# Optimization experiments

Hardware: AMD Instinct MI355X
Metric: run time of the kernel (lower is better)

Reference implementation:

```python
import jax, jax.numpy as jnp
import numpy as np
import math

B, LC, LQ, D = 64, 1024, 128, 128


def setup_inputs() -> dict:
    key = jax.random.key(0)
    k1, k2, k3, k4, k5 = jax.random.split(key, 5)
    c_rep = jax.random.normal(k1, (B, LC, D), dtype=jnp.float32)
    q_rep = jax.random.normal(k2, (B, LQ, D), dtype=jnp.float32)
    c_mask = jax.random.randint(k3, (B, LC), 0, 2, dtype=jnp.int32)
    q_mask = jax.random.randint(k4, (B, LQ), 0, 2, dtype=jnp.int32)
    lim = math.sqrt(1.0 / D)
    w = jax.random.uniform(k5, (3 * D,), dtype=jnp.float32, minval=-lim, maxval=lim)
    return {"c_rep": c_rep, "q_rep": q_rep, "c_mask": c_mask, "q_mask": q_mask, "w": w}


def _mask_logits(t, m):
    # mask == 1 means masked (matches original: target*(1-mask) + mask*-1e30)
    return t * (1.0 - m) + m * (-1e30)


def reference(c_rep, q_rep, c_mask, q_mask, w):
    d = c_rep.shape[-1]
    w1, w2, w3 = w[:d], w[d:2 * d], w[2 * d:]
    # Trilinear similarity S[b,i,j] = <ct,w1> + <qt,w2> + <ct*qt,w3>
    # computed without materializing the [B,Lc,Lq,3D] concat tensor.
    S = (c_rep @ w1)[:, :, None] \
        + (q_rep @ w2)[:, None, :] \
        + jnp.einsum('bid,bjd->bij', c_rep * w3, q_rep)  # [B, Lc, Lq]
    qm = q_mask[:, None, :].astype(S.dtype)  # [B, 1, Lq]
    cm = c_mask[:, :, None].astype(S.dtype)  # [B, Lc, 1]
    S1 = jax.nn.softmax(_mask_logits(S, qm), axis=2)  # softmax over query dim
    S2 = jax.nn.softmax(_mask_logits(S, cm), axis=1)  # softmax over context dim
    A = jnp.einsum('bij,bjd->bid', S1, q_rep)  # [B, Lc, D]
    # B_att = S1 @ S2^T @ c_rep, associated right-first to avoid [B,Lc,Lc]
    T = jnp.einsum('bkj,bkd->bjd', S2, c_rep)  # [B, Lq, D]
    B_att = jnp.einsum('bij,bjd->bid', S1, T)  # [B, Lc, D]
    out = jnp.concatenate([c_rep, A, c_rep * A, c_rep * B_att], axis=2)  # [B, Lc, 4D]
    # dropout is identity at inference
    return out
```

## Files before the change

### kernel.cpp

```cpp
#include <hip/hip_runtime.h>
#include <hip/hip_bf16.h>
#include <cstdint>
#include <cstddef>

#define B_   64
#define LC_  1024
#define LQ_  128
#define D_   128

typedef __bf16 bf16;
typedef bf16  bf16x8 __attribute__((ext_vector_type(8)));
typedef bf16  bf16x4 __attribute__((ext_vector_type(4)));
typedef float f32x4  __attribute__((ext_vector_type(4)));

__device__ __forceinline__ f32x4 mfma16(bf16x8 a, bf16x8 b, f32x4 c) {
  return __builtin_amdgcn_mfma_f32_16x16x32_bf16(a, b, c, 0, 0, 0);
}

__global__ __launch_bounds__(256) void k0c(const float* __restrict__ c, const float* __restrict__ w,
                                           float* __restrict__ cw1, bf16* __restrict__ cw3,
                                           bf16* __restrict__ cT) {
  __shared__ float w1s[128];
  __shared__ float w3s[128];
  __shared__ bf16  ctile[128 * 132];
  const int b = blockIdx.y, ks = blockIdx.x;
  const int k0 = ks * 128;
  const int t = threadIdx.x;
  if (t < 128) { w1s[t] = w[t]; w3s[t] = w[256 + t]; }
  __syncthreads();
  {
    const int r = t >> 1, d0 = (t & 1) * 64;
    const float* crow = c + ((size_t)(b * LC_ + k0 + r) * D_ + d0);
    bf16* orow = cw3 + ((size_t)(b * LC_ + k0 + r) * D_ + d0);
    float dot = 0.f;
#pragma unroll
    for (int v = 0; v < 8; ++v) {
      const float4 f0 = ((const float4*)crow)[v * 2 + 0];
      const float4 f1 = ((const float4*)crow)[v * 2 + 1];
      const int dd = d0 + v * 8;
      dot += f0.x * w1s[dd + 0] + f0.y * w1s[dd + 1] + f0.z * w1s[dd + 2] + f0.w * w1s[dd + 3]
           + f1.x * w1s[dd + 4] + f1.y * w1s[dd + 5] + f1.z * w1s[dd + 6] + f1.w * w1s[dd + 7];
      bf16* cr = &ctile[r * 132 + dd];
      cr[0] = (bf16)f0.x; cr[1] = (bf16)f0.y; cr[2] = (bf16)f0.z; cr[3] = (bf16)f0.w;
      cr[4] = (bf16)f1.x; cr[5] = (bf16)f1.y; cr[6] = (bf16)f1.z; cr[7] = (bf16)f1.w;
      bf16x8 o;
      o[0] = (bf16)(f0.x * w3s[dd + 0]); o[1] = (bf16)(f0.y * w3s[dd + 1]);
      o[2] = (bf16)(f0.z * w3s[dd + 2]); o[3] = (bf16)(f0.w * w3s[dd + 3]);
      o[4] = (bf16)(f1.x * w3s[dd + 4]); o[5] = (bf16)(f1.y * w3s[dd + 5]);
      o[6] = (bf16)(f1.z * w3s[dd + 6]); o[7] = (bf16)(f1.w * w3s[dd + 7]);
      *(bf16x8*)(orow + v * 8) = o;
    }
    dot += __shfl_xor(dot, 1);
    if ((t & 1) == 0) cw1[b * LC_ + k0 + r] = dot;
  }
  __syncthreads();
  {
    const int d = t >> 1, kh = (t & 1) * 64;
    bf16* trow = cT + ((size_t)(b * D_ + d) * LC_ + k0 + kh);
#pragma unroll
    for (int v = 0; v < 8; ++v) {
      bf16x8 o;
#pragma unroll
      for (int e = 0; e < 8; ++e) o[e] = ctile[(kh + v * 8 + e) * 132 + d];
      *(bf16x8*)(trow + v * 8) = o;
    }
  }
}

__global__ __launch_bounds__(256) void k0q(const float* __restrict__ q, const float* __restrict__ w,
                                           float* __restrict__ qw2, bf16* __restrict__ qb,
                                           bf16* __restrict__ qT) {
  __shared__ float w2s[128];
  __shared__ bf16  qtile[128 * 132];
  const int b = blockIdx.x;
  const int t = threadIdx.x;
  if (t < 128) w2s[t] = w[128 + t];
  __syncthreads();
  {
    const int r = t >> 1, d0 = (t & 1) * 64;
    const float* qrow = q + ((size_t)(b * LQ_ + r) * D_ + d0);
    bf16* orow = qb + ((size_t)(b * LQ_ + r) * D_ + d0);
    float dot = 0.f;
#pragma unroll
    for (int v = 0; v < 8; ++v) {
      const float4 f0 = ((const float4*)qrow)[v * 2 + 0];
      const float4 f1 = ((const float4*)qrow)[v * 2 + 1];
      const int dd = d0 + v * 8;
      dot += f0.x * w2s[dd + 0] + f0.y * w2s[dd + 1] + f0.z * w2s[dd + 2] + f0.w * w2s[dd + 3]
           + f1.x * w2s[dd + 4] + f1.y * w2s[dd + 5] + f1.z * w2s[dd + 6] + f1.w * w2s[dd + 7];
      bf16x8 o;
      o[0] = (bf16)f0.x; o[1] = (bf16)f0.y; o[2] = (bf16)f0.z; o[3] = (bf16)f0.w;
      o[4] = (bf16)f1.x; o[5] = (bf16)f1.y; o[6] = (bf16)f1.z; o[7] = (bf16)f1.w;
      bf16* qr = &qtile[r * 132 + dd];
#pragma unroll
      for (int e = 0; e < 8; ++e) qr[e] = o[e];
      *(bf16x8*)(orow + v * 8) = o;
    }
    dot += __shfl_xor(dot, 1);
    if ((t & 1) == 0) qw2[b * LQ_ + r] = dot;
  }
  __syncthreads();
  {
    const int d = t >> 1, jh = (t & 1) * 64;
    bf16* trow = qT + ((size_t)(b * D_ + d) * LQ_ + jh);
#pragma unroll
    for (int v = 0; v < 8; ++v) {
      bf16x8 o;
#pragma unroll
      for (int e = 0; e < 8; ++e) o[e] = qtile[(jh + v * 8 + e) * 132 + d];
      *(bf16x8*)(trow + v * 8) = o;
    }
  }
}

__global__ __launch_bounds__(256) void k1p(const float* __restrict__ cw1, const float* __restrict__ qw2,
                                           const int* __restrict__ cmask,
                                           const bf16* __restrict__ cw3, const bf16* __restrict__ cT,
                                           const bf16* __restrict__ qb,
                                           float* __restrict__ Tpart, float* __restrict__ lpart) {
  __shared__ bf16  qs[32 * 136];
  __shared__ bf16  cw3t[64 * 136];
  __shared__ bf16  cTt[128 * 72];
  __shared__ bf16  PT[32 * 72];
  __shared__ float lred[4][32];
  const int bx = blockIdx.x;
  const int ks = bx >> 2, js = bx & 3;
  const int b = blockIdx.y;
  const int j0 = js * 32;
  const int t = threadIdx.x;
  const int w = t >> 6, lane = t & 63, quad = lane >> 4, l15 = lane & 15;

#pragma unroll
  for (int idx = t; idx < 512; idx += 256) {
    const int row = idx >> 4, ch = idx & 15;
    *(bf16x8*)&qs[row * 136 + ch * 8] =
        *(const bf16x8*)(qb + ((size_t)(b * LQ_ + j0 + row) * D_ + ch * 8));
  }
  const f32x4 z = {0.f, 0.f, 0.f, 0.f};
  f32x4 Tacc[2][2] = {{z, z}, {z, z}};
  float lacc0 = 0.f, lacc1 = 0.f;
  __syncthreads();

  for (int kt = 0; kt < 8; ++kt) {
    const int k0g = ks * 512 + kt * 64;
#pragma unroll
    for (int idx = t; idx < 1024; idx += 256) {
      const int row = idx >> 4, ch = idx & 15;
      *(bf16x8*)&cw3t[row * 136 + ch * 8] =
          *(const bf16x8*)(cw3 + ((size_t)(b * LC_ + k0g + row) * D_ + ch * 8));
    }
#pragma unroll
    for (int idx = t; idx < 1024; idx += 256) {
      const int row = idx >> 3, ch = idx & 7;
      *(bf16x8*)&cTt[row * 72 + ch * 8] =
          *(const bf16x8*)(cT + ((size_t)(b * D_ + row) * LC_ + k0g + ch * 8));
    }
    __syncthreads();

    f32x4 S0 = z, S1 = z;
#pragma unroll
    for (int kk = 0; kk < 4; ++kk) {
      bf16x8 a  = *(bf16x8*)&cw3t[(w * 16 + l15) * 136 + kk * 32 + quad * 8];
      bf16x8 b0 = *(bf16x8*)&qs[l15 * 136 + kk * 32 + quad * 8];
      bf16x8 b1 = *(bf16x8*)&qs[(16 + l15) * 136 + kk * 32 + quad * 8];
      S0 = mfma16(a, b0, S0);
      S1 = mfma16(a, b1, S1);
    }
    const float qv0 = qw2[b * LQ_ + j0 + l15];
    const float qv1 = qw2[b * LQ_ + j0 + 16 + l15];
    bf16x4 pk0, pk1;
#pragma unroll
    for (int rr = 0; rr < 4; ++rr) {
      const int krow = k0g + w * 16 + quad * 4 + rr;
      const float c1 = cw1[b * LC_ + krow];
      const int   cm = cmask[b * LC_ + krow];
      const float p0 = cm ? 0.f : __expf(S0[rr] + c1 + qv0);
      const float p1 = cm ? 0.f : __expf(S1[rr] + c1 + qv1);
      lacc0 += p0; lacc1 += p1;
      pk0[rr] = (bf16)p0; pk1[rr] = (bf16)p1;
    }
    *(bf16x4*)&PT[l15 * 72 + w * 16 + quad * 4] = pk0;
    *(bf16x4*)&PT[(16 + l15) * 72 + w * 16 + quad * 4] = pk1;
    __syncthreads();

#pragma unroll
    for (int kk = 0; kk < 2; ++kk) {
      bf16x8 a0 = *(bf16x8*)&PT[l15 * 72 + kk * 32 + quad * 8];
      bf16x8 a1 = *(bf16x8*)&PT[(16 + l15) * 72 + kk * 32 + quad * 8];
      bf16x8 b0 = *(bf16x8*)&cTt[(w * 32 + l15) * 72 + kk * 32 + quad * 8];
      bf16x8 b1 = *(bf16x8*)&cTt[(w * 32 + 16 + l15) * 72 + kk * 32 + quad * 8];
      Tacc[0][0] = mfma16(a0, b0, Tacc[0][0]);
      Tacc[0][1] = mfma16(a0, b1, Tacc[0][1]);
      Tacc[1][0] = mfma16(a1, b0, Tacc[1][0]);
      Tacc[1][1] = mfma16(a1, b1, Tacc[1][1]);
    }
    __syncthreads();
  }

  lacc0 += __shfl_xor(lacc0, 16); lacc0 += __shfl_xor(lacc0, 32);
  lacc1 += __shfl_xor(lacc1, 16); lacc1 += __shfl_xor(lacc1, 32);
  if (lane < 16) { lred[w][l15] = lacc0; lred[w][16 + l15] = lacc1; }
  __syncthreads();
  if (t < 32)
    lpart[(size_t)(b * 2 + ks) * 128 + j0 + t] = lred[0][t] + lred[1][t] + lred[2][t] + lred[3][t];

  float* tp = Tpart + ((size_t)((b * 2 + ks) * 4 + js)) * (32 * 128);
#pragma unroll
  for (int mt = 0; mt < 2; ++mt)
#pragma unroll
    for (int nt = 0; nt < 2; ++nt)
#pragma unroll
      for (int rr = 0; rr < 4; ++rr)
        tp[(mt * 16 + quad * 4 + rr) * 128 + w * 32 + nt * 16 + l15] = Tacc[mt][nt][rr];
}

__global__ __launch_bounds__(256) void k1r(const float* __restrict__ Tpart,
                                           const float* __restrict__ lpart,
                                           bf16* __restrict__ TT) {
  __shared__ float Tsum[32 * 132];
  __shared__ float linv[32];
  const int js = blockIdx.x, b = blockIdx.y;
  const int j0 = js * 32;
  const int t = threadIdx.x;
  const float4* p0 = (const float4*)(Tpart + ((size_t)((b * 2 + 0) * 4 + js)) * (32 * 128));
  const float4* p1 = (const float4*)(Tpart + ((size_t)((b * 2 + 1) * 4 + js)) * (32 * 128));
#pragma unroll
  for (int idx = t; idx < 1024; idx += 256) {
    const int row = idx >> 5, seg = idx & 31;
    const float4 v0 = p0[idx];
    const float4 v1 = p1[idx];
    float4 s;
    s.x = v0.x + v1.x; s.y = v0.y + v1.y; s.z = v0.z + v1.z; s.w = v0.w + v1.w;
    *(float4*)&Tsum[row * 132 + seg * 4] = s;
  }
  if (t < 32)
    linv[t] = 1.f / (lpart[(size_t)(b * 2 + 0) * 128 + j0 + t] +
                     lpart[(size_t)(b * 2 + 1) * 128 + j0 + t]);
  __syncthreads();
  const int d = t >> 1, jh = (t & 1) * 16;
  bf16x8 o0, o1;
#pragma unroll
  for (int e = 0; e < 8; ++e) {
    o0[e] = (bf16)(Tsum[(jh + e) * 132 + d] * linv[jh + e]);
    o1[e] = (bf16)(Tsum[(jh + 8 + e) * 132 + d] * linv[jh + 8 + e]);
  }
  bf16* dst = TT + ((size_t)(b * D_ + d) * LQ_ + j0 + jh);
  *(bf16x8*)dst = o0;
  *(bf16x8*)(dst + 8) = o1;
}

__global__ __launch_bounds__(256) void k2(const float* __restrict__ c, const float* __restrict__ cw1,
                                          const float* __restrict__ qw2, const int* __restrict__ qmask,
                                          const bf16* __restrict__ cw3, const bf16* __restrict__ qb,
                                          const bf16* __restrict__ qT, const bf16* __restrict__ TT,
                                          float* __restrict__ out) {
  __shared__ __align__(16) char smem[51712];
  bf16* cw3i = (bf16*)(smem);
  bf16* qsl  = (bf16*)(smem + 17408);
  bf16* qTsl = (bf16*)(smem + 26112);
  bf16* TTsl = (bf16*)(smem + 36352);
  bf16* P1   = (bf16*)(smem + 46592);
  float* A32 = (float*)(smem);
  float* B32 = (float*)(smem + 16896);
  const int it = blockIdx.x, b = blockIdx.y;
  const int i0 = it * 64;
  const int t = threadIdx.x;
  const int w = t >> 6, lane = t & 63, quad = lane >> 4, l15 = lane & 15;

#pragma unroll
  for (int idx = t; idx < 1024; idx += 256) {
    const int row = idx >> 4, ch = idx & 15;
    *(bf16x8*)&cw3i[row * 136 + ch * 8] =
        *(const bf16x8*)(cw3 + ((size_t)(b * LC_ + i0 + row) * D_ + ch * 8));
  }
  const f32x4 z = {0.f, 0.f, 0.f, 0.f};
  f32x4 Aacc[8], Bacc[8];
#pragma unroll
  for (int n = 0; n < 8; ++n) { Aacc[n] = z; Bacc[n] = z; }
  float lacc[4] = {0.f, 0.f, 0.f, 0.f};
  __syncthreads();

  for (int jt = 0; jt < 4; ++jt) {
    const int j0 = jt * 32;
#pragma unroll
    for (int idx = t; idx < 512; idx += 256) {
      const int row = idx >> 4, ch = idx & 15;
      *(bf16x8*)&qsl[row * 136 + ch * 8] =
          *(const bf16x8*)(qb + ((size_t)(b * LQ_ + j0 + row) * D_ + ch * 8));
    }
#pragma unroll
    for (int idx = t; idx < 512; idx += 256) {
      const int row = idx >> 2, ch = idx & 3;
      *(bf16x8*)&qTsl[row * 40 + ch * 8] =
          *(const bf16x8*)(qT + ((size_t)(b * D_ + row) * LQ_ + j0 + ch * 8));
    }
#pragma unroll
    for (int idx = t; idx < 512; idx += 256) {
      const int row = idx >> 2, ch = idx & 3;
      *(bf16x8*)&TTsl[row * 40 + ch * 8] =
          *(const bf16x8*)(TT + ((size_t)(b * D_ + row) * LQ_ + j0 + ch * 8));
    }
    __syncthreads();

    f32x4 S0 = z, S1 = z;
#pragma unroll
    for (int kk = 0; kk < 4; ++kk) {
      bf16x8 a  = *(bf16x8*)&cw3i[(w * 16 + l15) * 136 + kk * 32 + quad * 8];
      bf16x8 b0 = *(bf16x8*)&qsl[l15 * 136 + kk * 32 + quad * 8];
      bf16x8 b1 = *(bf16x8*)&qsl[(16 + l15) * 136 + kk * 32 + quad * 8];
      S0 = mfma16(a, b0, S0);
      S1 = mfma16(a, b1, S1);
    }
    const float qv0 = qw2[b * LQ_ + j0 + l15];
    const float qv1 = qw2[b * LQ_ + j0 + 16 + l15];
    const int   qm0 = qmask[b * LQ_ + j0 + l15];
    const int   qm1 = qmask[b * LQ_ + j0 + 16 + l15];
#pragma unroll
    for (int rr = 0; rr < 4; ++rr) {
      const int irow = i0 + w * 16 + quad * 4 + rr;
      const float c1 = cw1[b * LC_ + irow];
      const float p0 = qm0 ? 0.f : __expf(S0[rr] + c1 + qv0);
      const float p1 = qm1 ? 0.f : __expf(S1[rr] + c1 + qv1);
      lacc[rr] += p0 + p1;
      P1[(w * 16 + quad * 4 + rr) * 40 + l15] = (bf16)p0;
      P1[(w * 16 + quad * 4 + rr) * 40 + 16 + l15] = (bf16)p1;
    }
    __syncthreads();

    bf16x8 aP = *(bf16x8*)&P1[(w * 16 + l15) * 40 + quad * 8];
#pragma unroll
    for (int nt = 0; nt < 8; ++nt) {
      bf16x8 bq = *(bf16x8*)&qTsl[(nt * 16 + l15) * 40 + quad * 8];
      bf16x8 bt = *(bf16x8*)&TTsl[(nt * 16 + l15) * 40 + quad * 8];
      Aacc[nt] = mfma16(aP, bq, Aacc[nt]);
      Bacc[nt] = mfma16(aP, bt, Bacc[nt]);
    }
    __syncthreads();
  }

#pragma unroll
  for (int rr = 0; rr < 4; ++rr) {
    float v = lacc[rr];
    v += __shfl_xor(v, 1); v += __shfl_xor(v, 2);
    v += __shfl_xor(v, 4); v += __shfl_xor(v, 8);
    lacc[rr] = 1.f / v;
  }

#pragma unroll
  for (int h = 0; h < 2; ++h) {
    if ((w >> 1) == h) {
      const int lrow0 = (w & 1) * 16 + quad * 4;
#pragma unroll
      for (int nt = 0; nt < 8; ++nt)
#pragma unroll
        for (int rr = 0; rr < 4; ++rr) {
          A32[(lrow0 + rr) * 132 + nt * 16 + l15] = Aacc[nt][rr] * lacc[rr];
          B32[(lrow0 + rr) * 132 + nt * 16 + l15] = Bacc[nt][rr] * lacc[rr];
        }
    }
    __syncthreads();
#pragma unroll
    for (int idx = t; idx < 1024; idx += 256) {
      const int lrow = idx >> 5, seg = idx & 31;
      const size_t grow = (size_t)(b * LC_ + i0 + h * 32 + lrow);
      const float4 c4 = ((const float4*)(c + grow * D_))[seg];
      const float4 a4 = *(float4*)&A32[lrow * 132 + seg * 4];
      const float4 b4 = *(float4*)&B32[lrow * 132 + seg * 4];
      float4* ob = (float4*)(out + grow * 512);
      ob[seg] = c4;
      ob[32 + seg] = a4;
      float4 ca; ca.x = c4.x * a4.x; ca.y = c4.y * a4.y; ca.z = c4.z * a4.z; ca.w = c4.w * a4.w;
      ob[64 + seg] = ca;
      float4 cb; cb.x = c4.x * b4.x; cb.y = c4.y * b4.y; cb.z = c4.z * b4.z; cb.w = c4.w * b4.w;
      ob[96 + seg] = cb;
    }
    __syncthreads();
  }
}

extern "C" void kernel_launch(void* const* d_in, const int* in_sizes, int n_in,
                              void* d_out, int out_size, void* d_ws, size_t ws_size,
                              hipStream_t stream) {
  (void)in_sizes; (void)n_in; (void)out_size; (void)ws_size;
  const float* c     = (const float*)d_in[0];
  const float* q     = (const float*)d_in[1];
  const int*   cmask = (const int*)d_in[2];
  const int*   qmask = (const int*)d_in[3];
  const float* w     = (const float*)d_in[4];
  float* out = (float*)d_out;

  char* ws = (char*)d_ws;
  float* cw1 = (float*)(ws + 0);
  float* qw2 = (float*)(ws + 262144);
  bf16*  cw3 = (bf16*)(ws + 294912);
  bf16*  cT  = (bf16*)(ws + 17072128);
  bf16*  qb  = (bf16*)(ws + 33849344);
  bf16*  qT  = (bf16*)(ws + 35946496);
  bf16*  TT  = (bf16*)(ws + 38043648);

  float* Tpart = out;
  float* lpart = out + 2097152;

  k0c<<<dim3(8, 64), 256, 0, stream>>>(c, w, cw1, cw3, cT);
  k0q<<<dim3(64), 256, 0, stream>>>(q, w, qw2, qb, qT);
  k1p<<<dim3(8, 64), 256, 0, stream>>>(cw1, qw2, cmask, cw3, cT, qb, Tpart, lpart);
  k1r<<<dim3(4, 64), 256, 0, stream>>>(Tpart, lpart, TT);
  k2<<<dim3(16, 64), 256, 0, stream>>>(c, cw1, qw2, qmask, cw3, qb, qT, TT, out);
}
```

Before: 245.8 us.

## Restructure k1p to cover all query columns per block with 4-way context split

k1p now has 512-thread blocks that each handle all 128 query columns, with the context dimension split into 4 chunks of 256 instead of 2 chunks × 4 query slices. This stops the cw3 and cT tiles from being reloaded once per query slice and gives each wave more MFMA work per shared-memory load. The reduction kernel k1r now sums four partials instead of two, and the partial buffers in the output scratch double in size. The trade-offs are half as many blocks in the grid (256), more shared memory per block, and more partial-sum traffic.

Result: faster. 237.7 us (-3.3%).

```diff
diff --git a/kernel.cpp b/kernel.cpp
--- a/kernel.cpp
+++ b/kernel.cpp
@@ -113,105 +113,116 @@
   }
 }
 
-__global__ __launch_bounds__(256) void k1p(const float* __restrict__ cw1, const float* __restrict__ qw2,
+__global__ __launch_bounds__(512) void k1p(const float* __restrict__ cw1, const float* __restrict__ qw2,
                                            const int* __restrict__ cmask,
                                            const bf16* __restrict__ cw3, const bf16* __restrict__ cT,
                                            const bf16* __restrict__ qb,
                                            float* __restrict__ Tpart, float* __restrict__ lpart) {
-  __shared__ bf16  qs[32 * 136];
+  __shared__ bf16  qs[128 * 136];
   __shared__ bf16  cw3t[64 * 136];
   __shared__ bf16  cTt[128 * 72];
-  __shared__ bf16  PT[32 * 72];
-  __shared__ float lred[4][32];
-  const int bx = blockIdx.x;
-  const int ks = bx >> 2, js = bx & 3;
-  const int b = blockIdx.y;
-  const int j0 = js * 32;
+  __shared__ bf16  PT[128 * 72];
+  __shared__ float lred[4][128];
+  const int ks = blockIdx.x, b = blockIdx.y;
   const int t = threadIdx.x;
   const int w = t >> 6, lane = t & 63, quad = lane >> 4, l15 = lane & 15;
-
-#pragma unroll
-  for (int idx = t; idx < 512; idx += 256) {
+  const int wk = w >> 1, wj = w & 1;
+
+#pragma unroll
+  for (int idx = t; idx < 2048; idx += 512) {
     const int row = idx >> 4, ch = idx & 15;
     *(bf16x8*)&qs[row * 136 + ch * 8] =
-        *(const bf16x8*)(qb + ((size_t)(b * LQ_ + j0 + row) * D_ + ch * 8));
+        *(const bf16x8*)(qb + ((size_t)(b * LQ_ + row) * D_ + ch * 8));
   }
   const f32x4 z = {0.f, 0.f, 0.f, 0.f};
-  f32x4 Tacc[2][2] = {{z, z}, {z, z}};
-  float lacc0 = 0.f, lacc1 = 0.f;
-  __syncthreads();
-
-  for (int kt = 0; kt < 8; ++kt) {
-    const int k0g = ks * 512 + kt * 64;
-#pragma unroll
-    for (int idx = t; idx < 1024; idx += 256) {
+  f32x4 Tacc[4][2];
+#pragma unroll
+  for (int jt = 0; jt < 4; ++jt) { Tacc[jt][0] = z; Tacc[jt][1] = z; }
+  float lacc[4] = {0.f, 0.f, 0.f, 0.f};
+  float qv[4];
+#pragma unroll
+  for (int jt = 0; jt < 4; ++jt) qv[jt] = qw2[b * LQ_ + wj * 64 + jt * 16 + l15];
+  __syncthreads();
+
+  for (int kt = 0; kt < 4; ++kt) {
+    const int k0g = ks * 256 + kt * 64;
+#pragma unroll
+    for (int idx = t; idx < 1024; idx += 512) {
       const int row = idx >> 4, ch = idx & 15;
       *(bf16x8*)&cw3t[row * 136 + ch * 8] =
           *(const bf16x8*)(cw3 + ((size_t)(b * LC_ + k0g + row) * D_ + ch * 8));
     }
 #pragma unroll
-    for (int idx = t; idx < 1024; idx += 256) {
+    for (int idx = t; idx < 1024; idx += 512) {
       const int row = idx >> 3, ch = idx & 7;
       *(bf16x8*)&cTt[row * 72 + ch * 8] =
           *(const bf16x8*)(cT + ((size_t)(b * D_ + row) * LC_ + k0g + ch * 8));
     }
     __syncthreads();
 
-    f32x4 S0 = z, S1 = z;
+    f32x4 S[4] = {z, z, z, z};
 #pragma unroll
     for (int kk = 0; kk < 4; ++kk) {
-      bf16x8 a  = *(bf16x8*)&cw3t[(w * 16 + l15) * 136 + kk * 32 + quad * 8];
-      bf16x8 b0 = *(bf16x8*)&qs[l15 * 136 + kk * 32 + quad * 8];
-      bf16x8 b1 = *(bf16x8*)&qs[(16 + l15) * 136 + kk * 32 + quad * 8];
-      S0 = mfma16(a, b0, S0);
-      S1 = mfma16(a, b1, S1);
-    }
-    const float qv0 = qw2[b * LQ_ + j0 + l15];
-    const float qv1 = qw2[b * LQ_ + j0 + 16 + l15];
-    bf16x4 pk0, pk1;
-#pragma unroll
-    for (int rr = 0; rr < 4; ++rr) {
-      const int krow = k0g + w * 16 + quad * 4 + rr;
-      const float c1 = cw1[b * LC_ + krow];
-      const int   cm = cmask[b * LC_ + krow];
-      const float p0 = cm ? 0.f : __expf(S0[rr] + c1 + qv0);
-      const float p1 = cm ? 0.f : __expf(S1[rr] + c1 + qv1);
-      lacc0 += p0; lacc1 += p1;
-      pk0[rr] = (bf16)p0; pk1[rr] = (bf16)p1;
-    }
-    *(bf16x4*)&PT[l15 * 72 + w * 16 + quad * 4] = pk0;
-    *(bf16x4*)&PT[(16 + l15) * 72 + w * 16 + quad * 4] = pk1;
+      bf16x8 a = *(bf16x8*)&cw3t[(wk * 16 + l15) * 136 + kk * 32 + quad * 8];
+#pragma unroll
+      for (int jt = 0; jt < 4; ++jt) {
+        bf16x8 bq = *(bf16x8*)&qs[(wj * 64 + jt * 16 + l15) * 136 + kk * 32 + quad * 8];
+        S[jt] = mfma16(a, bq, S[jt]);
+      }
+    }
+#pragma unroll
+    for (int jt = 0; jt < 4; ++jt) {
+      bf16x4 pk;
+#pragma unroll
+      for (int rr = 0; rr < 4; ++rr) {
+        const int krow = k0g + wk * 16 + quad * 4 + rr;
+        const float c1 = cw1[b * LC_ + krow];
+        const int   cm = cmask[b * LC_ + krow];
+        const float p = cm ? 0.f : __expf(S[jt][rr] + c1 + qv[jt]);
+        lacc[jt] += p;
+        pk[rr] = (bf16)p;
+      }
+      *(bf16x4*)&PT[(wj * 64 + jt * 16 + l15) * 72 + wk * 16 + quad * 4] = pk;
+    }
     __syncthreads();
 
 #pragma unroll
     for (int kk = 0; kk < 2; ++kk) {
-      bf16x8 a0 = *(bf16x8*)&PT[l15 * 72 + kk * 32 + quad * 8];
-      bf16x8 a1 = *(bf16x8*)&PT[(16 + l15) * 72 + kk * 32 + quad * 8];
-      bf16x8 b0 = *(bf16x8*)&cTt[(w * 32 + l15) * 72 + kk * 32 + quad * 8];
-      bf16x8 b1 = *(bf16x8*)&cTt[(w * 32 + 16 + l15) * 72 + kk * 32 + quad * 8];
-      Tacc[0][0] = mfma16(a0, b0, Tacc[0][0]);
-      Tacc[0][1] = mfma16(a0, b1, Tacc[0][1]);
-      Tacc[1][0] = mfma16(a1, b0, Tacc[1][0]);
-      Tacc[1][1] = mfma16(a1, b1, Tacc[1][1]);
-    }
-    __syncthreads();
-  }
-
-  lacc0 += __shfl_xor(lacc0, 16); lacc0 += __shfl_xor(lacc0, 32);
-  lacc1 += __shfl_xor(lacc1, 16); lacc1 += __shfl_xor(lacc1, 32);
-  if (lane < 16) { lred[w][l15] = lacc0; lred[w][16 + l15] = lacc1; }
-  __syncthreads();
-  if (t < 32)
-    lpart[(size_t)(b * 2 + ks) * 128 + j0 + t] = lred[0][t] + lred[1][t] + lred[2][t] + lred[3][t];
-
-  float* tp = Tpart + ((size_t)((b * 2 + ks) * 4 + js)) * (32 * 128);
-#pragma unroll
-  for (int mt = 0; mt < 2; ++mt)
-#pragma unroll
-    for (int nt = 0; nt < 2; ++nt)
+      bf16x8 bd0 = *(bf16x8*)&cTt[(wk * 32 + l15) * 72 + kk * 32 + quad * 8];
+      bf16x8 bd1 = *(bf16x8*)&cTt[(wk * 32 + 16 + l15) * 72 + kk * 32 + quad * 8];
+#pragma unroll
+      for (int jt = 0; jt < 4; ++jt) {
+        bf16x8 aP = *(bf16x8*)&PT[(wj * 64 + jt * 16 + l15) * 72 + kk * 32 + quad * 8];
+        Tacc[jt][0] = mfma16(aP, bd0, Tacc[jt][0]);
+        Tacc[jt][1] = mfma16(aP, bd1, Tacc[jt][1]);
+      }
+    }
+    __syncthreads();
+  }
+
+#pragma unroll
+  for (int jt = 0; jt < 4; ++jt) {
+    lacc[jt] += __shfl_xor(lacc[jt], 16);
+    lacc[jt] += __shfl_xor(lacc[jt], 32);
+  }
+  if (lane < 16) {
+#pragma unroll
+    for (int jt = 0; jt < 4; ++jt) lred[wk][wj * 64 + jt * 16 + l15] = lacc[jt];
+  }
+  __syncthreads();
+  if (t < 128)
+    lpart[(size_t)(b * 4 + ks) * 128 + t] =
+        lred[0][t] + lred[1][t] + lred[2][t] + lred[3][t];
+
+  float* tp = Tpart + ((size_t)(b * 4 + ks)) * (128 * 128);
+#pragma unroll
+  for (int jt = 0; jt < 4; ++jt)
+#pragma unroll
+    for (int dt = 0; dt < 2; ++dt)
 #pragma unroll
       for (int rr = 0; rr < 4; ++rr)
-        tp[(mt * 16 + quad * 4 + rr) * 128 + w * 32 + nt * 16 + l15] = Tacc[mt][nt][rr];
+        tp[(wj * 64 + jt * 16 + quad * 4 + rr) * 128 + wk * 32 + dt * 16 + l15] =
+            Tacc[jt][dt][rr];
 }
 
 __global__ __launch_bounds__(256) void k1r(const float* __restrict__ Tpart,
@@ -222,20 +233,29 @@
   const int js = blockIdx.x, b = blockIdx.y;
   const int j0 = js * 32;
   const int t = threadIdx.x;
-  const float4* p0 = (const float4*)(Tpart + ((size_t)((b * 2 + 0) * 4 + js)) * (32 * 128));
-  const float4* p1 = (const float4*)(Tpart + ((size_t)((b * 2 + 1) * 4 + js)) * (32 * 128));
+  const float4* p0 = (const float4*)(Tpart + ((size_t)(b * 4 + 0)) * (128 * 128)) + j0 * 32;
+  const float4* p1 = (const float4*)(Tpart + ((size_t)(b * 4 + 1)) * (128 * 128)) + j0 * 32;
+  const float4* p2 = (const float4*)(Tpart + ((size_t)(b * 4 + 2)) * (128 * 128)) + j0 * 32;
+  const float4* p3 = (const float4*)(Tpart + ((size_t)(b * 4 + 3)) * (128 * 128)) + j0 * 32;
 #pragma unroll
   for (int idx = t; idx < 1024; idx += 256) {
     const int row = idx >> 5, seg = idx & 31;
     const float4 v0 = p0[idx];
     const float4 v1 = p1[idx];
+    const float4 v2 = p2[idx];
+    const float4 v3 = p3[idx];
     float4 s;
-    s.x = v0.x + v1.x; s.y = v0.y + v1.y; s.z = v0.z + v1.z; s.w = v0.w + v1.w;
+    s.x = v0.x + v1.x + v2.x + v3.x;
+    s.y = v0.y + v1.y + v2.y + v3.y;
+    s.z = v0.z + v1.z + v2.z + v3.z;
+    s.w = v0.w + v1.w + v2.w + v3.w;
     *(float4*)&Tsum[row * 132 + seg * 4] = s;
   }
   if (t < 32)
-    linv[t] = 1.f / (lpart[(size_t)(b * 2 + 0) * 128 + j0 + t] +
-                     lpart[(size_t)(b * 2 + 1) * 128 + j0 + t]);
+    linv[t] = 1.f / (lpart[(size_t)(b * 4 + 0) * 128 + j0 + t] +
+                     lpart[(size_t)(b * 4 + 1) * 128 + j0 + t] +
+                     lpart[(size_t)(b * 4 + 2) * 128 + j0 + t] +
+                     lpart[(size_t)(b * 4 + 3) * 128 + j0 + t]);
   __syncthreads();
   const int d = t >> 1, jh = (t & 1) * 16;
   bf16x8 o0, o1;
@@ -399,11 +419,11 @@
   bf16*  TT  = (bf16*)(ws + 38043648);
 
   float* Tpart = out;
-  float* lpart = out + 2097152;
+  float* lpart = out + 4194304;
 
   k0c<<<dim3(8, 64), 256, 0, stream>>>(c, w, cw1, cw3, cT);
   k0q<<<dim3(64), 256, 0, stream>>>(q, w, qw2, qb, qT);
-  k1p<<<dim3(8, 64), 256, 0, stream>>>(cw1, qw2, cmask, cw3, cT, qb, Tpart, lpart);
+  k1p<<<dim3(4, 64), 512, 0, stream>>>(cw1, qw2, cmask, cw3, cT, qb, Tpart, lpart);
   k1r<<<dim3(4, 64), 256, 0, stream>>>(Tpart, lpart, TT);
   k2<<<dim3(16, 64), 256, 0, stream>>>(c, cw1, qw2, qmask, cw3, qb, qT, TT, out);
 }
```
